# Performance work log

Hardware: AMD Instinct MI355X
Metric: run time of the kernel (lower is better)

## Reference

```python
import jax, jax.numpy as jnp
import numpy as np

TEMPERATURE = 0.5
EPS = 1e-8  # F.cosine_similarity default eps
NEG_FILL = -1e9  # fill_diagonal_(-1000000000.0)


def setup_inputs() -> dict:
    key = jax.random.key(0)
    k1, k2 = jax.random.split(key)
    N, D = 4096, 256
    zi = jax.random.normal(k1, (N, D), dtype=jnp.float32)
    zj = jax.random.normal(k2, (N, D), dtype=jnp.float32)
    return {"zi": zi, "zj": zj}


def reference(zi, zj):
    N = zi.shape[0]
    z = jnp.concatenate([zi, zj], axis=0)  # [2N, D]
    # cosine similarity: normalize once, then a single GEMM
    norms = jnp.sqrt(jnp.sum(z * z, axis=1, keepdims=True))
    zn = z / jnp.maximum(norms, EPS)
    sim = jnp.matmul(zn, zn.T) / TEMPERATURE  # [2N, 2N]
    idx = jnp.arange(2 * N)
    sim = sim.at[idx, idx].set(NEG_FILL)  # mask self-similarity
    labels = jnp.concatenate([jnp.arange(N) + N, jnp.arange(N)])
    # CrossEntropyLoss(reduction='sum'): sum_i (logsumexp(row_i) - row_i[label_i])
    logp = jax.nn.log_softmax(sim, axis=1)
    loss = -jnp.sum(logp[idx, labels])
    return loss / (2 * N)
```

## Files before the change

kernel.cpp:

```cpp
#include <hip/hip_runtime.h>
#include <hip/hip_bf16.h>
#include <math.h>


using short8  = __attribute__((ext_vector_type(8))) short;
using floatx4 = __attribute__((ext_vector_type(4))) float;

constexpr int TWO_N = 8192;
constexpr int DIM   = 256;
constexpr int NB    = 64;
constexpr int NTRI  = NB * (NB + 1) / 2;
constexpr float INV2N = 1.0f / 8192.0f;

__device__ static inline unsigned short f2bf(float f) {
  unsigned u = __float_as_uint(f);
  return (unsigned short)((u + 0x7fffu + ((u >> 16) & 1u)) >> 16);
}

__device__ static inline void async_copy16(const __hip_bfloat16* g, __hip_bfloat16* l) {
  __builtin_amdgcn_global_load_lds(
      (const __attribute__((address_space(1))) void*)(const void*)g,
      (__attribute__((address_space(3))) void*)(void*)l, 16, 0, 0);
}

__global__ __launch_bounds__(256) void k_normalize(
    const float* __restrict__ zi, const float* __restrict__ zj,
    __hip_bfloat16* __restrict__ zn, float* __restrict__ rowtotal,
    float* __restrict__ out)
{
  if (blockIdx.x == 0 && threadIdx.x == 0) out[0] = 0.0f;
  if (blockIdx.x < 32) rowtotal[blockIdx.x * 256 + threadIdx.x] = 0.0f;

  const int lane = threadIdx.x & 63;
  const int wave = threadIdx.x >> 6;
  const int row  = blockIdx.x * 4 + wave;
  const float* src = (row < 4096) ? (zi + (size_t)row * DIM)
                                  : (zj + (size_t)(row - 4096) * DIM);
  float4 v = reinterpret_cast<const float4*>(src)[lane];
  float ss = v.x * v.x + v.y * v.y + v.z * v.z + v.w * v.w;
#pragma unroll
  for (int m = 32; m >= 1; m >>= 1) ss += __shfl_xor(ss, m, 64);
  float inv = 1.0f / fmaxf(sqrtf(ss), 1e-8f);
  ushort4 o;
  o.x = f2bf(v.x * inv); o.y = f2bf(v.y * inv);
  o.z = f2bf(v.z * inv); o.w = f2bf(v.w * inv);
  reinterpret_cast<ushort4*>(zn + (size_t)row * DIM)[lane] = o;
}

__global__ __launch_bounds__(256) void k_simexp(
    const __hip_bfloat16* __restrict__ Z, float* __restrict__ rowtotal,
    float* __restrict__ out)
{
  __shared__ __align__(16) __hip_bfloat16 As[128 * 64];
  __shared__ __align__(16) __hip_bfloat16 Bs[128 * 64];
  __shared__ float rowsum[128];
  __shared__ float colsum[128];

  const int tid  = threadIdx.x;
  const int lane = tid & 63;
  const int wave = tid >> 6;
  const int wm   = wave >> 1;
  const int wn   = wave & 1;

  const int u = blockIdx.x;
  int jb = (int)((sqrtf(8.0f * (float)u + 1.0f) - 1.0f) * 0.5f);
  while ((jb + 1) * (jb + 2) / 2 <= u) ++jb;
  while (jb * (jb + 1) / 2 > u) --jb;
  const int ib = u - jb * (jb + 1) / 2;

  const bool diagblk = (ib == jb);
  const bool pairblk = (jb == ib + 32);
  const int i0 = ib * 128;
  const int j0 = jb * 128;

  if (tid < 128) { rowsum[tid] = 0.0f; colsum[tid] = 0.0f; }

  floatx4 acc[4][4] = {};

  const int lane7 = lane & 7;
  const int sub   = lane >> 3;
  const int gkoff = ((lane7 ^ sub) << 3);
  const int q     = lane >> 4;
  const int c16   = lane & 15;

  const __hip_bfloat16* gbase =
      Z + (size_t)((wave < 2 ? i0 : j0) + (wave & 1) * 64) * DIM;
  __hip_bfloat16* lbase = ((wave < 2) ? As : Bs) + (wave & 1) * 64 * 64;

  for (int kk = 0; kk < 4; ++kk) {
    const int k0 = kk * 64;
#pragma unroll
    for (int c = 0; c < 8; ++c) {
      const __hip_bfloat16* gp = gbase + (size_t)(c * 8 + sub) * DIM + k0 + gkoff;
      async_copy16(gp, lbase + c * 512);
    }
    __syncthreads();

#pragma unroll
    for (int ks = 0; ks < 2; ++ks) {
      const int phys = (ks * 4 + q) ^ lane7;
      short8 a[4], b[4];
#pragma unroll
      for (int mt = 0; mt < 4; ++mt)
        a[mt] = *reinterpret_cast<const short8*>(
            As + (wm * 64 + mt * 16 + c16) * 64 + phys * 8);
#pragma unroll
      for (int nt = 0; nt < 4; ++nt)
        b[nt] = *reinterpret_cast<const short8*>(
            Bs + (wn * 64 + nt * 16 + c16) * 64 + phys * 8);
#pragma unroll
      for (int mt = 0; mt < 4; ++mt)
#pragma unroll
        for (int nt = 0; nt < 4; ++nt)
          acc[mt][nt] = __builtin_amdgcn_mfma_f32_16x16x32_bf16(
              a[mt], b[nt], acc[mt][nt], 0, 0, 0);
    }
    __syncthreads();
  }

  float colacc[4] = {0.f, 0.f, 0.f, 0.f};
  float pc = 0.f;
  const bool diagwave = (wm == wn);

#pragma unroll
  for (int mt = 0; mt < 4; ++mt) {
#pragma unroll
    for (int reg = 0; reg < 4; ++reg) {
      const bool onquad = (c16 == q * 4 + reg);
      float s = 0.0f;
#pragma unroll
      for (int nt = 0; nt < 4; ++nt) {
        float e = __expf(2.0f * acc[mt][nt][reg] - 2.0f);
        bool skip = diagblk && diagwave && (nt == mt) && onquad;
        s += skip ? 0.0f : e;
        colacc[nt] += e;
      }
      if (pairblk && diagwave && onquad) pc += acc[mt][mt][reg];
      s += __shfl_xor(s, 1, 64);
      s += __shfl_xor(s, 2, 64);
      s += __shfl_xor(s, 4, 64);
      s += __shfl_xor(s, 8, 64);
      if (c16 == 0)
        atomicAdd(&rowsum[wm * 64 + mt * 16 + q * 4 + reg], s);
    }
  }

  if (!diagblk) {
#pragma unroll
    for (int nt = 0; nt < 4; ++nt) {
      float cs = colacc[nt];
      cs += __shfl_xor(cs, 16, 64);
      cs += __shfl_xor(cs, 32, 64);
      if (lane < 16) atomicAdd(&colsum[wn * 64 + nt * 16 + lane], cs);
    }
  }

  if (pairblk && diagwave) {
#pragma unroll
    for (int m = 32; m >= 1; m >>= 1) pc += __shfl_xor(pc, m, 64);
    if (lane == 0) atomicAdd(out, -4.0f * pc * INV2N);
  }

  __syncthreads();
  if (tid < 128) {
    atomicAdd(&rowtotal[i0 + tid], rowsum[tid]);
    if (!diagblk) atomicAdd(&rowtotal[j0 + tid], colsum[tid]);
  }
}

__global__ __launch_bounds__(256) void k_finalize(
    const float* __restrict__ rowtotal, float* __restrict__ out)
{
  __shared__ float wsum[4];
  const int lane = threadIdx.x & 63;
  const int wave = threadIdx.x >> 6;
  const int row  = blockIdx.x * 256 + threadIdx.x;
  float v = 2.0f + __logf(rowtotal[row]);
#pragma unroll
  for (int m = 32; m >= 1; m >>= 1) v += __shfl_xor(v, m, 64);
  if (lane == 0) wsum[wave] = v;
  __syncthreads();
  if (threadIdx.x == 0)
    atomicAdd(out, (wsum[0] + wsum[1] + wsum[2] + wsum[3]) * INV2N);
}

extern "C" void kernel_launch(void* const* d_in, const int* in_sizes, int n_in,
                              void* d_out, int out_size, void* d_ws, size_t ws_size,
                              hipStream_t stream) {
  const float* zi = (const float*)d_in[0];
  const float* zj = (const float*)d_in[1];
  float* out = (float*)d_out;

  __hip_bfloat16* zn = (__hip_bfloat16*)d_ws;
  float* rowtotal = (float*)((char*)d_ws + (size_t)TWO_N * DIM * 2);

  k_normalize<<<dim3(TWO_N / 4), dim3(256), 0, stream>>>(zi, zj, zn, rowtotal, out);
  k_simexp<<<dim3(NTRI), dim3(256), 0, stream>>>(zn, rowtotal, out);
  k_finalize<<<dim3(TWO_N / 256), dim3(256), 0, stream>>>(rowtotal, out);
}
```

Measured before the change: 104.0 us.

## Remap block order across XCDs and replace row-sum shuffles with LDS scratch reduction

Block indices are permuted so consecutive hardware block ids map to strided triangular tiles, spreading neighbouring tiles across the chip's dies to change L2 locality and load balance. The per-row shuffle reductions and shared-memory atomics are replaced by writing partial row sums into a padded scratch array that aliases the GEMM tiles, then summing 32 partials per row serially. This removes many cross-lane shuffles and LDS atomics, but adds a serial 32-element loop for 128 threads and relies on the tile buffers no longer being needed after the final barrier.

```diff
diff --git a/kernel.cpp b/kernel.cpp
--- a/kernel.cpp
+++ b/kernel.cpp
@@ -51,10 +51,11 @@
     const __hip_bfloat16* __restrict__ Z, float* __restrict__ rowtotal,
     float* __restrict__ out)
 {
-  __shared__ __align__(16) __hip_bfloat16 As[128 * 64];
-  __shared__ __align__(16) __hip_bfloat16 Bs[128 * 64];
-  __shared__ float rowsum[128];
+  __shared__ __align__(16) char smem[128 * 64 * 2 * 2];
   __shared__ float colsum[128];
+  __hip_bfloat16* As = (__hip_bfloat16*)smem;
+  __hip_bfloat16* Bs = As + 128 * 64;
+  float* scratch = (float*)smem;
 
   const int tid  = threadIdx.x;
   const int lane = tid & 63;
@@ -62,7 +63,9 @@
   const int wm   = wave >> 1;
   const int wn   = wave & 1;
 
-  const int u = blockIdx.x;
+  const int bid = blockIdx.x;
+  const int u   = (bid & 7) * (NTRI / 8) + (bid >> 3);
+
   int jb = (int)((sqrtf(8.0f * (float)u + 1.0f) - 1.0f) * 0.5f);
   while ((jb + 1) * (jb + 2) / 2 <= u) ++jb;
   while (jb * (jb + 1) / 2 > u) --jb;
@@ -73,7 +76,7 @@
   const int i0 = ib * 128;
   const int j0 = jb * 128;
 
-  if (tid < 128) { rowsum[tid] = 0.0f; colsum[tid] = 0.0f; }
+  if (tid < 128) colsum[tid] = 0.0f;
 
   floatx4 acc[4][4] = {};
 
@@ -119,6 +122,7 @@
   }
 
   float colacc[4] = {0.f, 0.f, 0.f, 0.f};
+  float rowacc[4][4];
   float pc = 0.f;
   const bool diagwave = (wm == wn);
 
@@ -136,12 +140,7 @@
         colacc[nt] += e;
       }
       if (pairblk && diagwave && onquad) pc += acc[mt][mt][reg];
-      s += __shfl_xor(s, 1, 64);
-      s += __shfl_xor(s, 2, 64);
-      s += __shfl_xor(s, 4, 64);
-      s += __shfl_xor(s, 8, 64);
-      if (c16 == 0)
-        atomicAdd(&rowsum[wm * 64 + mt * 16 + q * 4 + reg], s);
+      rowacc[mt][reg] = s;
     }
   }
 
@@ -161,9 +160,20 @@
     if (lane == 0) atomicAdd(out, -4.0f * pc * INV2N);
   }
 
+#pragma unroll
+  for (int mt = 0; mt < 4; ++mt)
+#pragma unroll
+    for (int reg = 0; reg < 4; ++reg)
+      scratch[(wm * 64 + mt * 16 + q * 4 + reg) * 33 + wn * 16 + c16] =
+          rowacc[mt][reg];
+
   __syncthreads();
+
   if (tid < 128) {
-    atomicAdd(&rowtotal[i0 + tid], rowsum[tid]);
+    float rs = 0.0f;
+#pragma unroll
+    for (int k = 0; k < 32; ++k) rs += scratch[tid * 33 + k];
+    atomicAdd(&rowtotal[i0 + tid], rs);
     if (!diagblk) atomicAdd(&rowtotal[j0 + tid], colsum[tid]);
   }
 }
```

Result: faster. 90.16 us (-13.3%).
